# Optimization experiments

Measured on AMD Instinct MI355X. Metric: run time of the kernel, lower is better.

Reference implementation:

```python
import jax, jax.numpy as jnp
import numpy as np

B, N, E = 262144, 14, 12
THRESHOLD = 0.3


def setup_inputs() -> dict:
    key = jax.random.key(0)
    k1, k2 = jax.random.split(key)
    pos = jax.random.normal(k1, (B, N, 3), dtype=jnp.float32)
    rot = jax.random.normal(k2, (B, N, 9), dtype=jnp.float32)
    # two 7-node kinematic chains: left arm nodes 0..6, right arm nodes 7..13
    left = np.stack([np.arange(6), np.arange(1, 7)])
    right = np.stack([np.arange(7, 13), np.arange(8, 14)])
    edge_index = jnp.asarray(np.concatenate([left, right], axis=1), dtype=jnp.int32)  # [2, 12]
    ee_mask = jnp.zeros((N, 1), dtype=bool).at[6, 0].set(True).at[13, 0].set(True)
    return {"pos": pos, "rot": rot, "edge_index": edge_index, "ee_mask": ee_mask}


def _capsule_capsule_dist_square(p0, p1, q0, q1):
    # p*: [B, K, 3] left capsules (vary along axis j), q*: [B, K, 3] right capsules (vary along axis i)
    dp = p1 - p0                                  # [B, K, 3]
    dq = q1 - q0                                  # [B, K, 3]
    diff0 = p0[:, None, :, :] - q0[:, :, None, :]  # [B, K(i=q), K(j=p), 3]
    a = jnp.sum(dp * dp, -1)[:, None, :]          # [B, 1, K]
    c = jnp.sum(dq * dq, -1)[:, :, None]          # [B, K, 1]
    b = jnp.einsum('bjd,bid->bij', dp, dq)        # [B, K, K]
    d = jnp.sum(dp[:, None, :, :] * diff0, -1)
    e = jnp.sum(dq[:, :, None, :] * diff0, -1)
    det = a * c - b * b
    bte, ctd, ate, btd = b * e, c * d, a * e, b * d
    s = jnp.zeros_like(det)
    t = jnp.zeros_like(det)
    one = jnp.ones_like(det)
    s = jnp.where((det > 0) & (bte <= ctd) & (e <= 0) & (-d >= a), one, s)
    s = jnp.where((det > 0) & (bte <= ctd) & (e <= 0) & (-d < a) & (-d > 0), -d / a, s)
    t = jnp.where((det > 0) & (bte <= ctd) & (e > 0) & (e < c), e / c, t)
    s = jnp.where((det > 0) & (bte <= ctd) & (e > 0) & (e >= c) & (b - d >= a), one, s)
    s = jnp.where((det > 0) & (bte <= ctd) & (e > 0) & (e >= c) & (b - d < a) & (b - d > 0), (b - d) / a, s)
    t = jnp.where((det > 0) & (bte <= ctd) & (e > 0) & (e >= c), one, t)
    s = jnp.where((det > 0) & (bte > ctd) & (bte - ctd >= det) & (b + e <= 0) & (-d > 0) & (-d < a), -d / a, s)
    s = jnp.where((det > 0) & (bte > ctd) & (bte - ctd >= det) & (b + e <= 0) & (-d > 0) & (-d >= a), one, s)
    s = jnp.where((det > 0) & (bte > ctd) & (bte - ctd >= det) & (b + e > 0) & (b + e < c), one, s)
    t = jnp.where((det > 0) & (bte > ctd) & (bte - ctd >= det) & (b + e > 0) & (b + e < c), (b + e) / c, t)
    s = jnp.where((det > 0) & (bte > ctd) & (bte - ctd >= det) & (b + e > 0) & (b + e >= c) & (b - d > 0) & (b - d < a), (b - d) / a, s)
    s = jnp.where((det > 0) & (bte > ctd) & (bte - ctd >= det) & (b + e > 0) & (b + e >= c) & (b - d > 0) & (b - d >= a), one, s)
    t = jnp.where((det > 0) & (bte > ctd) & (bte - ctd >= det) & (b + e > 0) & (b + e >= c), one, t)
    s = jnp.where((det > 0) & (bte > ctd) & (bte - ctd < det) & (ate <= btd) & (-d > 0) & (-d >= a), one, s)
    s = jnp.where((det > 0) & (bte > ctd) & (bte - ctd < det) & (ate <= btd) & (-d > 0) & (-d < a), -d / a, s)
    s = jnp.where((det > 0) & (bte > ctd) & (bte - ctd < det) & (ate > btd) & (ate - btd >= det) & (b - d > 0) & (b - d >= a), one, s)
    s = jnp.where((det > 0) & (bte > ctd) & (bte - ctd < det) & (ate > btd) & (ate - btd >= det) & (b - d > 0) & (b - d < a), (b - d) / a, s)
    t = jnp.where((det > 0) & (bte > ctd) & (bte - ctd < det) & (ate > btd) & (ate - btd >= det), one, t)
    s = jnp.where((det > 0) & (bte > ctd) & (bte - ctd < det) & (ate > btd) & (ate - btd < det), (bte - ctd) / det, s)
    t = jnp.where((det > 0) & (bte > ctd) & (bte - ctd < det) & (ate > btd) & (ate - btd < det), (ate - btd) / det, t)
    s = jnp.where((det <= 0) & (e <= 0) & (-d > 0) & (-d >= a), one, s)
    s = jnp.where((det <= 0) & (e <= 0) & (-d > 0) & (-d < a), -d / a, s)
    s = jnp.where((det <= 0) & (e > 0) & (e >= c) & (b - d > 0) & (b - d >= a), one, s)
    s = jnp.where((det <= 0) & (e > 0) & (e >= c) & (b - d > 0) & (b - d < a), (b - d) / a, s)
    t = jnp.where((det <= 0) & (e > 0) & (e >= c), one, t)
    t = jnp.where((det <= 0) & (e > 0) & (e < c), e / c, t)
    # original code detaches s and t before forming w
    s = jax.lax.stop_gradient(s)
    t = jax.lax.stop_gradient(t)
    w = diff0 + s[..., None] * dp[:, None, :, :] - t[..., None] * dq[:, :, None, :]
    return jnp.sum(w * w, -1)  # [B, K, K]


def reference(pos, rot, edge_index, ee_mask):
    bsz, n_nodes = pos.shape[0], pos.shape[1]
    n_edges = edge_index.shape[1]
    half = n_edges // 2
    p0 = pos[:, edge_index[0]]  # [B, E, 3]
    p1 = pos[:, edge_index[1]]
    l_p0, r_p0 = p0[:, :half], p0[:, half:]
    l_p1, r_p1 = p1[:, :half], p1[:, half:]
    # exactly 2 end-effectors (left, right) marked in ee_mask
    ee_idx = jnp.nonzero(ee_mask[:, 0], size=2)[0]
    ee_pos = pos[:, ee_idx]                         # [B, 2, 3]  (left, right)
    ee_rot = rot[:, ee_idx].reshape(bsz, 2, 3, 3)   # [B, 2, 3, 3]
    offset = jnp.array([0.0, 0.0, 0.2], dtype=pos.dtype)
    hand_pos = jnp.einsum('beij,j->bei', ee_rot, offset) + ee_pos  # [B, 2, 3]
    l_p0 = jnp.concatenate([l_p0, ee_pos[:, 0:1]], axis=1)   # [B, E/2+1, 3]
    l_p1 = jnp.concatenate([l_p1, hand_pos[:, 0:1]], axis=1)
    r_p0 = jnp.concatenate([r_p0, ee_pos[:, 1:2]], axis=1)
    r_p1 = jnp.concatenate([r_p1, hand_pos[:, 1:2]], axis=1)
    dist_square = _capsule_capsule_dist_square(l_p0, l_p1, r_p0, r_p1)  # [B, 7, 7]
    mask = (dist_square < 0.1 ** 2) & (dist_square > 0)
    special = (dist_square[:, 6, 6] > THRESHOLD ** 2) & (dist_square[:, 6, 6] > 0)
    mask = mask.at[:, 6, 6].set(special)
    loss = jnp.sum(jnp.where(mask, jnp.exp(-dist_square), jnp.zeros_like(dist_square))) / bsz
    return loss
```

## Files before the change

kernel.cpp:

```cpp
#include <hip/hip_runtime.h>


__device__ __forceinline__ float rcpf(float x) { return __builtin_amdgcn_rcpf(x); }
__device__ __forceinline__ float clamp01(float x) {
    return __builtin_amdgcn_fmed3f(x, 0.0f, 1.0f);
}

__device__ __forceinline__ float cap_dist2(
    float px0, float py0, float pz0, float px1, float py1, float pz1,
    float qx0, float qy0, float qz0, float qx1, float qy1, float qz1)
{
    const float dpx = px1 - px0, dpy = py1 - py0, dpz = pz1 - pz0;
    const float dqx = qx1 - qx0, dqy = qy1 - qy0, dqz = qz1 - qz0;
    const float rx  = px0 - qx0, ry  = py0 - qy0, rz  = pz0 - qz0;

    const float a = dpx*dpx + dpy*dpy + dpz*dpz;
    const float c = dqx*dqx + dqy*dqy + dqz*dqz;
    const float b = dpx*dqx + dpy*dqy + dpz*dqz;
    const float d = dpx*rx + dpy*ry + dpz*rz;
    const float e = dqx*rx + dqy*ry + dqz*rz;
    const float det = a*c - b*b;

    const float rcp_a = rcpf(a);
    const float rcp_c = rcpf(c);

    const float f  = b*e - c*d;
    const float s0 = (det > 0.0f) ? clamp01(f * rcpf(det)) : 0.0f;

    const float tn = b*s0 + e;
    const float t  = clamp01(tn * rcp_c);

    const float sA = clamp01(-d * rcp_a);
    const float sB = clamp01((b - d) * rcp_a);
    const float s  = (tn < 0.0f) ? sA : ((tn > c) ? sB : s0);

    const float wx = rx + s*dpx - t*dqx;
    const float wy = ry + s*dpy - t*dqy;
    const float wz = rz + s*dpz - t*dqz;
    return wx*wx + wy*wy + wz*wz;
}

#define BT 128

__global__ __launch_bounds__(BT) void collision_loss_kernel(
    const float* __restrict__ pos,
    const float* __restrict__ rot,
    float* __restrict__ out)
{
    __shared__ float2 sbuf[BT * 21 + 8];
    __shared__ float wsum[2];

    const int tid       = threadIdx.x;
    const int blockBase = blockIdx.x * BT;
    const int b         = blockBase + tid;

    const float* rb = rot + (size_t)b * 126;
    const float r6x = rb[ 56], r6y = rb[ 59], r6z = rb[ 62];
    const float rdx = rb[119], rdy = rb[122], rdz = rb[125];

    const float2* g2 = reinterpret_cast<const float2*>(pos + (size_t)blockBase * 42);
    #pragma unroll
    for (int k = 0; k < 21; ++k) {
        const int idx = k * BT + tid;
        sbuf[idx] = g2[idx];
    }
    __syncthreads();

    const float2* m2 = sbuf + tid * 21;
    const float*  mf = reinterpret_cast<const float*>(sbuf) + tid * 42;
    const float2 u0 = m2[0], u1 = m2[1], u2 = m2[2], u3 = m2[3], u4 = m2[4];
    const float2 u5 = m2[5], u6 = m2[6], u7 = m2[7], u8 = m2[8], u9 = m2[9];
    const float n6z = mf[20];

    const float n0x=u0.x, n0y=u0.y, n0z=u1.x;
    const float n1x=u1.y, n1y=u2.x, n1z=u2.y;
    const float n2x=u3.x, n2y=u3.y, n2z=u4.x;
    const float n3x=u4.y, n3y=u5.x, n3z=u5.y;
    const float n4x=u6.x, n4y=u6.y, n4z=u7.x;
    const float n5x=u7.y, n5y=u8.x, n5z=u8.y;
    const float n6x=u9.x, n6y=u9.y;

    const float hlx = n6x + 0.2f * r6x;
    const float hly = n6y + 0.2f * r6y;
    const float hlz = n6z + 0.2f * r6z;

    float q0x = mf[21], q0y = mf[22], q0z = mf[23];

    float sum = 0.0f;

    auto acc = [&](float p0x, float p0y, float p0z,
                   float p1x, float p1y, float p1z,
                   float q0x_, float q0y_, float q0z_,
                   float q1x_, float q1y_, float q1z_, bool special) {
        const float d2 = cap_dist2(p0x,p0y,p0z, p1x,p1y,p1z,
                                   q0x_,q0y_,q0z_, q1x_,q1y_,q1z_);
        const bool m = special ? (d2 > 0.09f)
                               : ((d2 < 0.01f) && (d2 > 0.0f));
        sum += m ? __expf(-d2) : 0.0f;
    };

    #pragma unroll 1
    for (int i = 0; i < 7; ++i) {
        const int base = 24 + 3 * i;
        const float lx = mf[base], ly = mf[base + 1], lz = mf[base + 2];
        const bool last = (i == 6);
        const float q1x = last ? fmaf(0.2f, rdx, q0x) : lx;
        const float q1y = last ? fmaf(0.2f, rdy, q0y) : ly;
        const float q1z = last ? fmaf(0.2f, rdz, q0z) : lz;

        acc(n0x,n0y,n0z, n1x,n1y,n1z, q0x,q0y,q0z, q1x,q1y,q1z, false);
        acc(n1x,n1y,n1z, n2x,n2y,n2z, q0x,q0y,q0z, q1x,q1y,q1z, false);
        acc(n2x,n2y,n2z, n3x,n3y,n3z, q0x,q0y,q0z, q1x,q1y,q1z, false);
        acc(n3x,n3y,n3z, n4x,n4y,n4z, q0x,q0y,q0z, q1x,q1y,q1z, false);
        acc(n4x,n4y,n4z, n5x,n5y,n5z, q0x,q0y,q0z, q1x,q1y,q1z, false);
        acc(n5x,n5y,n5z, n6x,n6y,n6z, q0x,q0y,q0z, q1x,q1y,q1z, false);
        acc(n6x,n6y,n6z, hlx,hly,hlz, q0x,q0y,q0z, q1x,q1y,q1z, last);

        q0x = q1x; q0y = q1y; q0z = q1z;
    }

    #pragma unroll
    for (int off = 32; off > 0; off >>= 1)
        sum += __shfl_down(sum, off, 64);
    const int wave = tid >> 6;
    if ((tid & 63) == 0) wsum[wave] = sum;
    __syncthreads();
    if (tid == 0) {
        atomicAdd(out, (wsum[0] + wsum[1]) * (1.0f / 262144.0f));
    }
}

extern "C" void kernel_launch(void* const* d_in, const int* in_sizes, int n_in,
                              void* d_out, int out_size, void* d_ws, size_t ws_size,
                              hipStream_t stream) {
    const float* pos = (const float*)d_in[0];
    const float* rot = (const float*)d_in[1];
    float* out = (float*)d_out;

    const int B = in_sizes[0] / 42;
    hipMemsetAsync(out, 0, sizeof(float), stream);

    collision_loss_kernel<<<B / BT, BT, 0, stream>>>(pos, rot, out);
}
```

Before: 221.1 us.

## Split each batch's capsule pairs across seven waves, one right capsule per wave

Each block now handles 64 batch items with 448 threads, and each of the seven waves computes the seven left-capsule distances against one right capsule. Before, one thread looped over all 49 pairs for its batch item. The rot end-effector entries are gathered cooperatively into shared memory instead of being loaded per thread with strided accesses. This gives seven times more threads and a shorter serial chain per thread, in exchange for redundant loads of the left-arm data in each wave, more shared-memory reads, and a larger block reduction.

```diff
diff --git a/kernel.cpp b/kernel.cpp
--- a/kernel.cpp
+++ b/kernel.cpp
@@ -40,34 +40,43 @@
     return wx*wx + wy*wy + wz*wz;
 }
 
-#define BT 128
+#define BT   448
+#define BPB  64
 
 __global__ __launch_bounds__(BT) void collision_loss_kernel(
     const float* __restrict__ pos,
     const float* __restrict__ rot,
     float* __restrict__ out)
 {
-    __shared__ float2 sbuf[BT * 21 + 8];
-    __shared__ float wsum[2];
+    __shared__ float slab[BPB * 42];
+    __shared__ float aux [BPB * 6];
+    __shared__ float wsum[7];
 
     const int tid       = threadIdx.x;
-    const int blockBase = blockIdx.x * BT;
-    const int b         = blockBase + tid;
-
-    const float* rb = rot + (size_t)b * 126;
-    const float r6x = rb[ 56], r6y = rb[ 59], r6z = rb[ 62];
-    const float rdx = rb[119], rdy = rb[122], rdz = rb[125];
+    const int blockBase = blockIdx.x * BPB;
 
     const float2* g2 = reinterpret_cast<const float2*>(pos + (size_t)blockBase * 42);
+    float2*       s2 = reinterpret_cast<float2*>(slab);
     #pragma unroll
-    for (int k = 0; k < 21; ++k) {
+    for (int k = 0; k < 3; ++k) {
         const int idx = k * BT + tid;
-        sbuf[idx] = g2[idx];
+        s2[idx] = g2[idx];
+    }
+
+    if (tid < BPB * 6) {
+        const int batch = tid / 6;
+        const int comp  = tid - 6 * batch;
+        const int off   = (comp < 3) ? (56 + 3 * comp) : (110 + 3 * comp);
+        aux[tid] = rot[(size_t)(blockBase + batch) * 126 + off];
     }
     __syncthreads();
 
-    const float2* m2 = sbuf + tid * 21;
-    const float*  mf = reinterpret_cast<const float*>(sbuf) + tid * 42;
+    const int w = tid >> 6;
+    const int l = tid & 63;
+
+    const float2* m2 = reinterpret_cast<const float2*>(slab) + l * 21;
+    const float*  mf = slab + l * 42;
+    const float*  ax = aux  + l * 6;
     const float2 u0 = m2[0], u1 = m2[1], u2 = m2[2], u3 = m2[3], u4 = m2[4];
     const float2 u5 = m2[5], u6 = m2[6], u7 = m2[7], u8 = m2[8], u9 = m2[9];
     const float n6z = mf[20];
@@ -80,53 +89,49 @@
     const float n5x=u7.y, n5y=u8.x, n5z=u8.y;
     const float n6x=u9.x, n6y=u9.y;
 
-    const float hlx = n6x + 0.2f * r6x;
-    const float hly = n6y + 0.2f * r6y;
-    const float hlz = n6z + 0.2f * r6z;
+    const float hlx = n6x + 0.2f * ax[0];
+    const float hly = n6y + 0.2f * ax[1];
+    const float hlz = n6z + 0.2f * ax[2];
 
-    float q0x = mf[21], q0y = mf[22], q0z = mf[23];
+    const int qb = 21 + 3 * w;
+    const float q0x = mf[qb], q0y = mf[qb + 1], q0z = mf[qb + 2];
+    float q1x, q1y, q1z;
+    if (w < 6) {
+        q1x = mf[qb + 3]; q1y = mf[qb + 4]; q1z = mf[qb + 5];
+    } else {
+        q1x = q0x + 0.2f * ax[3];
+        q1y = q0y + 0.2f * ax[4];
+        q1z = q0z + 0.2f * ax[5];
+    }
 
     float sum = 0.0f;
 
     auto acc = [&](float p0x, float p0y, float p0z,
-                   float p1x, float p1y, float p1z,
-                   float q0x_, float q0y_, float q0z_,
-                   float q1x_, float q1y_, float q1z_, bool special) {
+                   float p1x, float p1y, float p1z, bool special) {
         const float d2 = cap_dist2(p0x,p0y,p0z, p1x,p1y,p1z,
-                                   q0x_,q0y_,q0z_, q1x_,q1y_,q1z_);
+                                   q0x,q0y,q0z, q1x,q1y,q1z);
         const bool m = special ? (d2 > 0.09f)
                                : ((d2 < 0.01f) && (d2 > 0.0f));
         sum += m ? __expf(-d2) : 0.0f;
     };
 
-    #pragma unroll 1
-    for (int i = 0; i < 7; ++i) {
-        const int base = 24 + 3 * i;
-        const float lx = mf[base], ly = mf[base + 1], lz = mf[base + 2];
-        const bool last = (i == 6);
-        const float q1x = last ? fmaf(0.2f, rdx, q0x) : lx;
-        const float q1y = last ? fmaf(0.2f, rdy, q0y) : ly;
-        const float q1z = last ? fmaf(0.2f, rdz, q0z) : lz;
-
-        acc(n0x,n0y,n0z, n1x,n1y,n1z, q0x,q0y,q0z, q1x,q1y,q1z, false);
-        acc(n1x,n1y,n1z, n2x,n2y,n2z, q0x,q0y,q0z, q1x,q1y,q1z, false);
-        acc(n2x,n2y,n2z, n3x,n3y,n3z, q0x,q0y,q0z, q1x,q1y,q1z, false);
-        acc(n3x,n3y,n3z, n4x,n4y,n4z, q0x,q0y,q0z, q1x,q1y,q1z, false);
-        acc(n4x,n4y,n4z, n5x,n5y,n5z, q0x,q0y,q0z, q1x,q1y,q1z, false);
-        acc(n5x,n5y,n5z, n6x,n6y,n6z, q0x,q0y,q0z, q1x,q1y,q1z, false);
-        acc(n6x,n6y,n6z, hlx,hly,hlz, q0x,q0y,q0z, q1x,q1y,q1z, last);
-
-        q0x = q1x; q0y = q1y; q0z = q1z;
-    }
+    acc(n0x,n0y,n0z, n1x,n1y,n1z, false);
+    acc(n1x,n1y,n1z, n2x,n2y,n2z, false);
+    acc(n2x,n2y,n2z, n3x,n3y,n3z, false);
+    acc(n3x,n3y,n3z, n4x,n4y,n4z, false);
+    acc(n4x,n4y,n4z, n5x,n5y,n5z, false);
+    acc(n5x,n5y,n5z, n6x,n6y,n6z, false);
+    acc(n6x,n6y,n6z, hlx,hly,hlz, w == 6);
 
     #pragma unroll
     for (int off = 32; off > 0; off >>= 1)
         sum += __shfl_down(sum, off, 64);
-    const int wave = tid >> 6;
-    if ((tid & 63) == 0) wsum[wave] = sum;
+    if (l == 0) wsum[w] = sum;
     __syncthreads();
     if (tid == 0) {
-        atomicAdd(out, (wsum[0] + wsum[1]) * (1.0f / 262144.0f));
+        const float s = ((wsum[0] + wsum[1]) + (wsum[2] + wsum[3]))
+                      + ((wsum[4] + wsum[5]) + wsum[6]);
+        atomicAdd(out, s * (1.0f / 262144.0f));
     }
 }
 
@@ -140,5 +145,5 @@
     const int B = in_sizes[0] / 42;
     hipMemsetAsync(out, 0, sizeof(float), stream);
 
-    collision_loss_kernel<<<B / BT, BT, 0, stream>>>(pos, rot, out);
+    collision_loss_kernel<<<B / BPB, BT, 0, stream>>>(pos, rot, out);
 }
```

Result: slower. 228.6 us (+3.4%).
